# Optimization experiments

Hardware: AMD Instinct MI355X
Metric: run time of the kernel (lower is better)

Reference implementation:

```python
import jax, jax.numpy as jnp
import numpy as np

HEADS = 8
EPS = 1e-12  # F.normalize default eps


def conv1x1(t, w):
    # t: (B, Cin, H, W); w: (Cout, Cin) -> (B, Cout, H, W)
    return jnp.einsum('bchw,oc->bohw', t, w)


def cosine_attn(q, k, v, scale):
    # q: (B,h,d,Nq); k,v: (B,h,d,Nk). Cosine attention: L2-normalize over feature dim d.
    q = q / jnp.maximum(jnp.linalg.norm(q, axis=2, keepdims=True), EPS)
    k = k / jnp.maximum(jnp.linalg.norm(k, axis=2, keepdims=True), EPS)
    attn = jnp.einsum('bhdq,bhdk->bhqk', q, k) * scale
    attn = jax.nn.softmax(attn, axis=-1)
    return jnp.einsum('bhqk,bhdk->bhdq', attn, v)  # (B,h,d,Nq)


def setup_inputs() -> dict:
    key = jax.random.key(0)
    ks = jax.random.split(key, 8)
    B, C, H, W, L = 8, 512, 64, 64, 16
    def w(k, o, i):
        return jax.random.normal(k, (o, i), dtype=jnp.float32) * (1.0 / np.sqrt(i))
    return {
        'x': jax.random.normal(ks[0], (B, C, H, W), dtype=jnp.float32),
        'latents': jax.random.normal(ks[1], (1, C, 1, L), dtype=jnp.float32) * 0.02,
        'w_q_lat': w(ks[2], C, C),
        'w_kv_x': w(ks[3], 2 * C, C),
        'w_q_x': w(ks[4], C, C),
        'w_kv_lat': w(ks[5], 2 * C, C),
        'w_proj': w(ks[6], C, C),
        'b_proj': jnp.zeros((C,), dtype=jnp.float32),
    }


def reference(x, latents, w_q_lat, w_kv_x, w_q_x, w_kv_lat, w_proj, b_proj):
    B, C, H, W = x.shape
    L = latents.shape[-1]
    h = HEADS
    d = C // h
    scale = d ** (-0.5)

    # latents read from spatial features (compression)
    lat = jnp.broadcast_to(latents, (B, C, 1, L))
    ql = conv1x1(lat, w_q_lat).reshape(B, h, d, L)
    kvx = conv1x1(x, w_kv_x)
    kx = kvx[:, :C].reshape(B, h, d, H * W)
    vx = kvx[:, C:].reshape(B, h, d, H * W)
    lat_read = cosine_attn(ql, kx, vx, scale).reshape(B, C, 1, L)

    # latents write back into features (expansion)
    qx = conv1x1(x, w_q_x).reshape(B, h, d, H * W)
    kvl = conv1x1(lat_read, w_kv_lat)
    kl = kvl[:, :C].reshape(B, h, d, L)
    vl = kvl[:, C:].reshape(B, h, d, L)
    x_write = cosine_attn(qx, kl, vl, scale).reshape(B, C, H, W)

    # output projection (dropout p=0 -> identity)
    return conv1x1(x_write, w_proj) + b_proj[None, :, None, None]
```

## Files before the change

kernel.cpp:

```cpp
#include <hip/hip_runtime.h>


typedef __bf16 bf16x8 __attribute__((ext_vector_type(8)));
typedef float floatx4 __attribute__((ext_vector_type(4)));
typedef short short8_t __attribute__((ext_vector_type(8)));
typedef short short4_t __attribute__((ext_vector_type(4)));

#define DEV __device__ __forceinline__

DEV float bf2f(unsigned short u){ union{unsigned int i; float f;} v; v.i = ((unsigned int)u)<<16; return v.f; }
DEV unsigned short f2bf(float f){
  union{float f; unsigned int i;} v; v.f = f;
  unsigned int i = v.i;
  return (unsigned short)((i + 0x7fffu + ((i>>16)&1u)) >> 16);
}

#define OFF_XT     256ull
#define OFF_KVX    (OFF_XT + 33554432ull)
#define OFF_WKVX   (OFF_KVX + 67108864ull)
#define OFF_WQX    (OFF_WKVX + 1048576ull)
#define OFF_WKVL   (OFF_WQX + 524288ull)
#define OFF_WPROJ  (OFF_WKVL + 1048576ull)
#define OFF_WQLAT  (OFF_WPROJ + 524288ull)
#define OFF_LATF   (OFF_WQLAT + 524288ull)
#define OFF_BIAS   (OFF_LATF + 32768ull)
#define OFF_QL     (OFF_BIAS + 4096ull)
#define OFF_QLH    (OFF_QL + 32768ull)
#define OFF_GNUM   (OFF_QLH + 32768ull)
#define OFF_GDEN   (OFF_GNUM + 524288ull)
#define OFF_KVL    (OFF_GDEN + 4096ull)
#define OFF_KHAT   (OFF_KVL + 524288ull)
#define OFF_GVL    (OFF_KHAT + 524288ull)

__global__ void k_sniff(const unsigned short* __restrict__ x, int* flag){
  int t = threadIdx.x;
  int m = 0;
  for (int i = t; i < 4096; i += 256){ int e = (x[i]>>7)&0xFF; m = (e>m)?e:m; }
  __shared__ int red[256];
  red[t] = m; __syncthreads();
  for (int s = 128; s > 0; s >>= 1){ if (t < s) red[t] = (red[t+s]>red[t])?red[t+s]:red[t]; __syncthreads(); }
  if (t == 0) flag[0] = (red[0] > 150) ? 1 : 0;
}

__global__ __launch_bounds__(256) void k_cvt(const void* __restrict__ src, unsigned short* __restrict__ dst,
                                             int n, const int* __restrict__ flag){
  int base = (blockIdx.x*256 + threadIdx.x)*8;
  if (base >= n) return;
  if (*flag){
    const float* s = (const float*)src + base;
    float4 v0 = *(const float4*)(s);
    float4 v1 = *(const float4*)(s+4);
    unsigned short tmp[8] __attribute__((aligned(16)));
    tmp[0]=f2bf(v0.x); tmp[1]=f2bf(v0.y); tmp[2]=f2bf(v0.z); tmp[3]=f2bf(v0.w);
    tmp[4]=f2bf(v1.x); tmp[5]=f2bf(v1.y); tmp[6]=f2bf(v1.z); tmp[7]=f2bf(v1.w);
    *(short8_t*)&dst[base] = *(short8_t*)tmp;
  } else {
    *(short8_t*)&dst[base] = *(const short8_t*)((const unsigned short*)src + base);
  }
}

__global__ void k_cvtf(const void* __restrict__ src, float* __restrict__ dst, int n, const int* __restrict__ flag){
  int i = blockIdx.x*256 + threadIdx.x;
  if (i >= n) return;
  dst[i] = (*flag) ? ((const float*)src)[i] : bf2f(((const unsigned short*)src)[i]);
}

__global__ __launch_bounds__(256) void k_xt(const void* __restrict__ xraw, unsigned short* __restrict__ xT,
                                            const int* __restrict__ flag){
  int nb = blockIdx.x, cb = blockIdx.y, b = blockIdx.z;
  int n0 = nb*64, c0 = cb*64;
  __shared__ unsigned short tile[64][72];
  int t = threadIdx.x;
  if (*flag){
    const float* xp = (const float*)xraw;
#pragma unroll
    for (int i = 0; i < 4; ++i){
      int ch = i*256 + t; int c = ch>>4, n4 = (ch&15)*4;
      float4 v = *(const float4*)&xp[((size_t)(b*512 + c0 + c))*4096 + n0 + n4];
      int cc = n4 ^ (((c>>3)&7)<<3);
      tile[c][cc+0]=f2bf(v.x); tile[c][cc+1]=f2bf(v.y); tile[c][cc+2]=f2bf(v.z); tile[c][cc+3]=f2bf(v.w);
    }
  } else {
    const unsigned short* xp = (const unsigned short*)xraw;
#pragma unroll
    for (int i = 0; i < 2; ++i){
      int ch = i*256 + t; int c = ch>>3, n8 = (ch&7)*8;
      *(short8_t*)&tile[c][n8 ^ (((c>>3)&7)<<3)] =
        *(const short8_t*)&xp[((size_t)(b*512 + c0 + c))*4096 + n0 + n8];
    }
  }
  __syncthreads();
#pragma unroll
  for (int i = 0; i < 2; ++i){
    int ch = i*256 + t; int n = ch>>3, c8 = (ch&7)*8;
    unsigned short tmp[8] __attribute__((aligned(16)));
#pragma unroll
    for (int j = 0; j < 8; ++j){
      int c = c8 + j;
      tmp[j] = tile[c][n ^ (((c>>3)&7)<<3)];
    }
    *(short8_t*)&xT[((size_t)(b*4096 + n0 + n))*512 + c0 + c8] = *(short8_t*)tmp;
  }
}

__global__ __launch_bounds__(256) void k_ql(const unsigned short* __restrict__ wqlat,
                                            const float* __restrict__ latf, float* __restrict__ ql){
  int o0 = blockIdx.x*64;
  extern __shared__ char smr[];
  float* latb = (float*)smr;
  unsigned short* wt = (unsigned short*)(smr + 8192);
  int t = threadIdx.x;
  int o = t>>2, l4 = (t&3)*4;
  float acc[4] = {0.f,0.f,0.f,0.f};
  for (int kk = 0; kk < 512; kk += 128){
    __syncthreads();
#pragma unroll
    for (int j = 0; j < 8; ++j){ int i = j*256 + t; latb[i] = latf[kk*16 + i]; }
#pragma unroll
    for (int j = 0; j < 4; ++j){ int ch = j*256 + t; int r = ch>>4, kc = (ch&15)*8;
      *(short8_t*)&wt[r*136 + kc] = *(const short8_t*)&wqlat[(size_t)(o0+r)*512 + kk + kc]; }
    __syncthreads();
    for (int k = 0; k < 128; ++k){
      float w = bf2f(wt[o*136 + k]);
      const float* lr = &latb[k*16 + l4];
#pragma unroll
      for (int j = 0; j < 4; ++j) acc[j] += w*lr[j];
    }
  }
#pragma unroll
  for (int j = 0; j < 4; ++j) ql[(o0+o)*16 + l4 + j] = acc[j];
}

__global__ void k_qlnorm(const float* __restrict__ ql, float* __restrict__ qlh){
  int l = blockIdx.x, h = blockIdx.y, d = threadIdx.x;
  float v = ql[(h*64 + d)*16 + l];
  float ss = v*v;
  for (int off = 32; off; off >>= 1) ss += __shfl_xor(ss, off);
  qlh[(h*16 + l)*64 + d] = 0.125f * v / fmaxf(sqrtf(ss), 1e-12f);
}

DEV void gemm128(const unsigned short* __restrict__ Ap0, const unsigned short* __restrict__ Ap1,
                 const unsigned short* __restrict__ Bp,
                 unsigned short* At, unsigned short* Bt, floatx4 (&acc)[4][4]){
  int t = threadIdx.x, lane = t&63, wave = t>>6;
  int wm = wave>>1, wn = wave&1, lr = lane&15, lq = lane>>4;
  for (int kk = 0; kk < 512; kk += 64){
    __syncthreads();
#pragma unroll
    for (int i = 0; i < 4; ++i){
      int ch = i*256 + t; int r = ch>>3, kc = (ch&7)*8;
      const unsigned short* ap = (i < 2) ? (Ap0 + (size_t)r*512) : (Ap1 + (size_t)(r-64)*512);
      *(short8_t*)&At[r*72 + kc] = *(const short8_t*)&ap[kk + kc];
    }
#pragma unroll
    for (int i = 0; i < 4; ++i){
      int ch = i*256 + t; int r = ch>>3, kc = (ch&7)*8;
      *(short8_t*)&Bt[r*72 + kc] = *(const short8_t*)&Bp[(size_t)r*512 + kk + kc];
    }
    __syncthreads();
#pragma unroll
    for (int ks = 0; ks < 2; ++ks){
      bf16x8 a[4], b[4];
#pragma unroll
      for (int mt = 0; mt < 4; ++mt) a[mt] = *(const bf16x8*)&At[(wm*64 + mt*16 + lr)*72 + ks*32 + lq*8];
#pragma unroll
      for (int nt = 0; nt < 4; ++nt) b[nt] = *(const bf16x8*)&Bt[(wn*64 + nt*16 + lr)*72 + ks*32 + lq*8];
#pragma unroll
      for (int mt = 0; mt < 4; ++mt)
#pragma unroll
        for (int nt = 0; nt < 4; ++nt)
          acc[mt][nt] = __builtin_amdgcn_mfma_f32_16x16x32_bf16(a[mt], b[nt], acc[mt][nt], 0, 0, 0);
    }
  }
  __syncthreads();
}

__global__ __launch_bounds__(256) void k_kvattn1(const unsigned short* __restrict__ wkvx,
                                                 const unsigned short* __restrict__ xT,
                                                 const float* __restrict__ qlh2,
                                                 float* __restrict__ gnum, float* __restrict__ gden){
  int nb = blockIdx.x, h = blockIdx.y, b = blockIdx.z;
  int n0 = nb*128;
  extern __shared__ char smr[];
  unsigned short* At  = (unsigned short*)smr;
  unsigned short* Bt  = At + 128*72;
  unsigned short* kt  = At;
  unsigned short* vt  = Bt;
  unsigned short* qls = (unsigned short*)(smr + 36864);
  float* ssq  = (float*)(smr + 39168);
  float* wred = (float*)(smr + 39680);
  unsigned short* pt  = (unsigned short*)(smr + 39936);
  int t = threadIdx.x, lane = t&63, wave = t>>6;
  int wm = wave>>1, wn = wave&1, lr = lane&15, lq = lane>>4;
  floatx4 acc[4][4];
  floatx4 zero = {0.f,0.f,0.f,0.f};
#pragma unroll
  for (int i = 0; i < 4; ++i) for (int j = 0; j < 4; ++j) acc[i][j] = zero;
  gemm128(wkvx + (size_t)(h*64)*512, wkvx + (size_t)(512 + h*64)*512,
          xT + ((size_t)(b*4096 + n0))*512, At, Bt, acc);
  for (int i = t; i < 1024; i += 256) qls[(i>>6)*72 + (i&63)] = f2bf(qlh2[(size_t)h*1024 + i]);
  if (wm == 0){
#pragma unroll
    for (int nt = 0; nt < 4; ++nt){
      float s = 0.f;
#pragma unroll
      for (int mt = 0; mt < 4; ++mt)
#pragma unroll
        for (int r = 0; r < 4; ++r) s += acc[mt][nt][r]*acc[mt][nt][r];
      s += __shfl_xor(s, 16); s += __shfl_xor(s, 32);
      if (lq == 0) ssq[wn*64 + nt*16 + lr] = 1.f / fmaxf(sqrtf(s), 1e-12f);
    }
  } else {
#pragma unroll
    for (int mt = 0; mt < 4; ++mt)
#pragma unroll
      for (int nt = 0; nt < 4; ++nt){
        int col = wn*64 + nt*16 + lr;
#pragma unroll
        for (int r = 0; r < 4; ++r) vt[(mt*16 + lq*4 + r)*136 + col] = f2bf(acc[mt][nt][r]);
      }
  }
  __syncthreads();
  if (wm == 0){
#pragma unroll
    for (int nt = 0; nt < 4; ++nt){
      int col = wn*64 + nt*16 + lr;
      float rinv = ssq[col];
#pragma unroll
      for (int mt = 0; mt < 4; ++mt){
        unsigned short tmp[4] __attribute__((aligned(8)));
#pragma unroll
        for (int r = 0; r < 4; ++r) tmp[r] = f2bf(acc[mt][nt][r]*rinv);
        *(short4_t*)&kt[col*72 + mt*16 + lq*4] = *(short4_t*)tmp;
      }
    }
  }
  __syncthreads();
  floatx4 sl[2]; sl[0] = zero; sl[1] = zero;
#pragma unroll
  for (int ks = 0; ks < 2; ++ks){
    bf16x8 bb = *(const bf16x8*)&qls[lr*72 + ks*32 + lq*8];
#pragma unroll
    for (int i = 0; i < 2; ++i){
      bf16x8 aa = *(const bf16x8*)&kt[((wave*2 + i)*16 + lr)*72 + ks*32 + lq*8];
      sl[i] = __builtin_amdgcn_mfma_f32_16x16x32_bf16(aa, bb, sl[i], 0, 0, 0);
    }
  }
  float dp = 0.f;
  float pv[2][4];
#pragma unroll
  for (int i = 0; i < 2; ++i)
#pragma unroll
    for (int r = 0; r < 4; ++r){ float p = __expf(sl[i][r]); pv[i][r] = p; dp += p; }
  dp += __shfl_xor(dp, 16); dp += __shfl_xor(dp, 32);
  if (lq == 0) wred[wave*16 + lr] = dp;
#pragma unroll
  for (int i = 0; i < 2; ++i){
    unsigned short tmp[4] __attribute__((aligned(8)));
#pragma unroll
    for (int r = 0; r < 4; ++r) tmp[r] = f2bf(pv[i][r]);
    *(short4_t*)&pt[lr*136 + (wave*2 + i)*16 + lq*4] = *(short4_t*)tmp;
  }
  __syncthreads();
  int bh = b*8 + h;
  if (t < 16) atomicAdd(&gden[bh*16 + t], wred[t] + wred[16+t] + wred[32+t] + wred[48+t]);
  floatx4 nacc = zero;
#pragma unroll
  for (int ks = 0; ks < 4; ++ks){
    bf16x8 aa = *(const bf16x8*)&vt[(wave*16 + lr)*136 + ks*32 + lq*8];
    bf16x8 bb = *(const bf16x8*)&pt[lr*136 + ks*32 + lq*8];
    nacc = __builtin_amdgcn_mfma_f32_16x16x32_bf16(aa, bb, nacc, 0, 0, 0);
  }
  float* gp = &gnum[((size_t)bh*16 + lr)*64 + wave*16 + lq*4];
#pragma unroll
  for (int r = 0; r < 4; ++r) atomicAdd(&gp[r], nacc[r]);
}

__global__ __launch_bounds__(256) void k_kvl(const unsigned short* __restrict__ wkvl,
                                             const float* __restrict__ gnum, const float* __restrict__ gden,
                                             float* __restrict__ kvl){
  int ob = blockIdx.x, b = blockIdx.y;
  extern __shared__ char smr[];
  float* latb = (float*)smr;
  unsigned short* wt = (unsigned short*)(smr + 32768);
  int t = threadIdx.x;
  for (int i = t; i < 8192; i += 256){
    int c = i>>4, l = i&15;
    int h = c>>6, d = c&63;
    int bh = b*8 + h;
    latb[i] = gnum[((size_t)(bh*16 + l))*64 + d] / gden[bh*16 + l];
  }
  int o = t>>4, l = t&15;
  int o0 = ob*16;
  float acc = 0.f;
  for (int kk = 0; kk < 512; kk += 128){
    __syncthreads();
    { int r = t>>4, kc = (t&15)*8;
      *(short8_t*)&wt[r*136 + kc] = *(const short8_t*)&wkvl[(size_t)(o0+r)*512 + kk + kc]; }
    __syncthreads();
    for (int k = 0; k < 128; ++k) acc += bf2f(wt[o*136 + k]) * latb[(kk+k)*16 + l];
  }
  kvl[((size_t)(b*1024 + o0 + o))*16 + l] = acc;
}

__global__ void k_klnorm(const float* __restrict__ kvl, float* __restrict__ khat, float* __restrict__ gvl){
  int l = blockIdx.x, h = blockIdx.y, b = blockIdx.z, d = threadIdx.x;
  float kl = kvl[((size_t)(b*1024 + h*64 + d))*16 + l];
  float vl = kvl[((size_t)(b*1024 + 512 + h*64 + d))*16 + l];
  float ss = kl*kl;
  for (int off = 32; off; off >>= 1) ss += __shfl_xor(ss, off);
  float inv = 0.125f / fmaxf(sqrtf(ss), 1e-12f);
  size_t o = ((size_t)((b*8+h)*16 + l))*64 + d;
  khat[o] = kl*inv;
  gvl[o] = vl;
}

__global__ __launch_bounds__(256) void k_mmat(const unsigned short* __restrict__ wproj,
                                              const float* __restrict__ gvl,
                                              unsigned short* __restrict__ Mg){
  int cb = blockIdx.x, h = blockIdx.y, b = blockIdx.z;
  __shared__ unsigned short wt[128*68];
  int t = threadIdx.x;
#pragma unroll
  for (int i = 0; i < 4; ++i){ int ch = i*256 + t; int c = ch>>3, d8 = (ch&7)*8;
    *(short8_t*)&wt[c*68 + d8] = *(const short8_t*)&wproj[(size_t)(cb*128 + c)*512 + h*64 + d8]; }
  int l = t&15, cq = t>>4;
  float v[64];
  const float* vp = &gvl[((size_t)(b*8+h)*16 + l)*64];
#pragma unroll
  for (int j = 0; j < 16; ++j){ float4 f = *(const float4*)&vp[j*4];
    v[j*4+0]=f.x; v[j*4+1]=f.y; v[j*4+2]=f.z; v[j*4+3]=f.w; }
  __syncthreads();
#pragma unroll
  for (int c8 = 0; c8 < 8; ++c8){
    int c = cq*8 + c8;
    float dot = 0.f;
#pragma unroll
    for (int d = 0; d < 64; ++d) dot += bf2f(wt[c*68 + d]) * v[d];
    Mg[((size_t)(b*512) + cb*128 + c)*128 + h*16 + l] = f2bf(dot);
  }
}

__global__ __launch_bounds__(256) void k_attn2p2(const unsigned short* __restrict__ wqx,
                                                 const unsigned short* __restrict__ xT,
                                                 const float* __restrict__ khatg,
                                                 unsigned short* __restrict__ Pg){
  int nb = blockIdx.x, hp = blockIdx.y, b = blockIdx.z;
  int n0 = nb*128;
  extern __shared__ char smr[];
  unsigned short* At  = (unsigned short*)smr;
  unsigned short* Bt  = At + 128*72;
  unsigned short* qt0 = At;
  unsigned short* qt1 = Bt;
  unsigned short* khs = (unsigned short*)(smr + 36864);
  float* ssq = (float*)(smr + 41472);
  int t = threadIdx.x, lane = t&63, wave = t>>6;
  int wm = wave>>1, wn = wave&1, lr = lane&15, lq = lane>>4;
  floatx4 acc[4][4];
  floatx4 zero = {0.f,0.f,0.f,0.f};
#pragma unroll
  for (int i = 0; i < 4; ++i) for (int j = 0; j < 4; ++j) acc[i][j] = zero;
  gemm128(wqx + (size_t)(hp*128)*512, wqx + (size_t)(hp*128 + 64)*512,
          xT + ((size_t)(b*4096 + n0))*512, At, Bt, acc);
  for (int i = t; i < 2048; i += 256){
    int hh = i>>10, rem = i&1023;
    khs[hh*1152 + (rem>>6)*72 + (rem&63)] = f2bf(khatg[((size_t)(b*8 + hp*2 + hh))*1024 + rem]);
  }
#pragma unroll
  for (int nt = 0; nt < 4; ++nt){
    float s = 0.f;
#pragma unroll
    for (int mt = 0; mt < 4; ++mt)
#pragma unroll
      for (int r = 0; r < 4; ++r) s += acc[mt][nt][r]*acc[mt][nt][r];
    s += __shfl_xor(s, 16); s += __shfl_xor(s, 32);
    if (lq == 0) ssq[wm*128 + wn*64 + nt*16 + lr] = 1.f / fmaxf(sqrtf(s), 1e-12f);
  }
  __syncthreads();
  unsigned short* qtr = wm ? qt1 : qt0;
#pragma unroll
  for (int nt = 0; nt < 4; ++nt){
    int col = wn*64 + nt*16 + lr;
    float rinv = ssq[wm*128 + col];
#pragma unroll
    for (int mt = 0; mt < 4; ++mt){
      unsigned short tmp[4] __attribute__((aligned(8)));
#pragma unroll
      for (int r = 0; r < 4; ++r) tmp[r] = f2bf(acc[mt][nt][r]*rinv);
      *(short4_t*)&qtr[col*72 + mt*16 + lq*4] = *(short4_t*)tmp;
    }
  }
  __syncthreads();
  floatx4 sl[4];
#pragma unroll
  for (int i = 0; i < 4; ++i) sl[i] = zero;
#pragma unroll
  for (int ks = 0; ks < 2; ++ks){
    bf16x8 bb = *(const bf16x8*)&khs[wm*1152 + lr*72 + ks*32 + lq*8];
#pragma unroll
    for (int i = 0; i < 4; ++i){
      bf16x8 aa = *(const bf16x8*)&qtr[((wn*4 + i)*16 + lr)*72 + ks*32 + lq*8];
      sl[i] = __builtin_amdgcn_mfma_f32_16x16x32_bf16(aa, bb, sl[i], 0, 0, 0);
    }
  }
  int h = hp*2 + wm;
#pragma unroll
  for (int i = 0; i < 4; ++i){
    float p[4], s[4];
#pragma unroll
    for (int r = 0; r < 4; ++r){ p[r] = __expf(sl[i][r]); s[r] = p[r]; }
#pragma unroll
    for (int r = 0; r < 4; ++r){
      s[r] += __shfl_xor(s[r], 1);
      s[r] += __shfl_xor(s[r], 2);
      s[r] += __shfl_xor(s[r], 4);
      s[r] += __shfl_xor(s[r], 8);
    }
    int nbase = wn*64 + i*16 + lq*4;
#pragma unroll
    for (int r = 0; r < 4; ++r)
      Pg[((size_t)(b*4096 + n0 + nbase + r))*128 + h*16 + lr] = f2bf(p[r]/s[r]);
  }
}

__global__ __launch_bounds__(256) void k_out(const unsigned short* __restrict__ Mg,
                                             const unsigned short* __restrict__ Pg,
                                             const float* __restrict__ biasf,
                                             void* __restrict__ outv, const int* __restrict__ flag){
  int nb = blockIdx.x, cb = blockIdx.y, b = blockIdx.z;
  int n0 = nb*128, c0 = cb*64;
  extern __shared__ char smr[];
  unsigned short* At = (unsigned short*)smr;
  unsigned short* Bt = At + 64*136;
  int t = threadIdx.x, lane = t&63, wave = t>>6;
  int wm = wave>>1, wn = wave&1, lr = lane&15, lq = lane>>4;
#pragma unroll
  for (int i = 0; i < 4; ++i){ int ch = i*256 + t; int r = ch>>4, p8 = (ch&15)*8;
    *(short8_t*)&At[r*136 + p8] = *(const short8_t*)&Mg[((size_t)(b*512 + c0 + r))*128 + p8]; }
#pragma unroll
  for (int i = 0; i < 8; ++i){ int ch = i*256 + t; int r = ch>>4, p8 = (ch&15)*8;
    *(short8_t*)&Bt[r*136 + p8] = *(const short8_t*)&Pg[((size_t)(b*4096 + n0 + r))*128 + p8]; }
  __syncthreads();
  floatx4 acc[2][4];
  floatx4 zero = {0.f,0.f,0.f,0.f};
#pragma unroll
  for (int i = 0; i < 2; ++i) for (int j = 0; j < 4; ++j) acc[i][j] = zero;
#pragma unroll
  for (int ks = 0; ks < 4; ++ks){
    bf16x8 a0 = *(const bf16x8*)&At[(wm*32 + lr)*136 + ks*32 + lq*8];
    bf16x8 a1 = *(const bf16x8*)&At[(wm*32 + 16 + lr)*136 + ks*32 + lq*8];
#pragma unroll
    for (int nt = 0; nt < 4; ++nt){
      bf16x8 bb = *(const bf16x8*)&Bt[(wn*64 + nt*16 + lr)*136 + ks*32 + lq*8];
      acc[0][nt] = __builtin_amdgcn_mfma_f32_16x16x32_bf16(a0, bb, acc[0][nt], 0, 0, 0);
      acc[1][nt] = __builtin_amdgcn_mfma_f32_16x16x32_bf16(a1, bb, acc[1][nt], 0, 0, 0);
    }
  }
  __syncthreads();
  float* ct = (float*)smr;
#pragma unroll
  for (int mt = 0; mt < 2; ++mt)
#pragma unroll
    for (int nt = 0; nt < 4; ++nt)
#pragma unroll
      for (int r = 0; r < 4; ++r){
        int row = wm*32 + mt*16 + lq*4 + r;
        ct[row*132 + wn*64 + nt*16 + lr] = acc[mt][nt][r] + biasf[c0 + row];
      }
  __syncthreads();
  if (*flag){
    float* of = (float*)outv;
#pragma unroll
    for (int i = 0; i < 8; ++i){ int ch = i*256 + t; int r = ch>>5, c4 = (ch&31)*4;
      *(float4*)&of[((size_t)(b*512 + c0 + r))*4096 + n0 + c4] = *(float4*)&ct[r*132 + c4]; }
  } else {
    unsigned short* ob = (unsigned short*)outv;
#pragma unroll
    for (int i = 0; i < 4; ++i){ int ch = i*256 + t; int r = ch>>4, c8 = (ch&15)*8;
      unsigned short tmp[8] __attribute__((aligned(16)));
#pragma unroll
      for (int j = 0; j < 8; ++j) tmp[j] = f2bf(ct[r*132 + c8 + j]);
      *(short8_t*)&ob[((size_t)(b*512 + c0 + r))*4096 + n0 + c8] = *(short8_t*)tmp; }
  }
}

extern "C" void kernel_launch(void* const* d_in, const int* in_sizes, int n_in,
                              void* d_out, int out_size, void* d_ws, size_t ws_size,
                              hipStream_t stream){
  (void)in_sizes; (void)n_in; (void)out_size; (void)ws_size;
  char* ws = (char*)d_ws;
  int* flag              = (int*)ws;
  unsigned short* xT     = (unsigned short*)(ws + OFF_XT);
  unsigned short* Pg     = (unsigned short*)(ws + OFF_KVX);
  unsigned short* Mg     = (unsigned short*)(ws + OFF_KVX + 8388608ull);
  unsigned short* wkvx   = (unsigned short*)(ws + OFF_WKVX);
  unsigned short* wqx    = (unsigned short*)(ws + OFF_WQX);
  unsigned short* wkvl   = (unsigned short*)(ws + OFF_WKVL);
  unsigned short* wproj  = (unsigned short*)(ws + OFF_WPROJ);
  unsigned short* wqlat  = (unsigned short*)(ws + OFF_WQLAT);
  float* latf  = (float*)(ws + OFF_LATF);
  float* biasf = (float*)(ws + OFF_BIAS);
  float* ql    = (float*)(ws + OFF_QL);
  float* qlh   = (float*)(ws + OFF_QLH);
  float* gnum  = (float*)(ws + OFF_GNUM);
  float* gden  = (float*)(ws + OFF_GDEN);
  float* kvl   = (float*)(ws + OFF_KVL);
  float* khat  = (float*)(ws + OFF_KHAT);
  float* gvl   = (float*)(ws + OFF_GVL);

  k_sniff<<<1, 256, 0, stream>>>((const unsigned short*)d_in[0], flag);

  k_cvt<<<256, 256, 0, stream>>>(d_in[3], wkvx, 524288, flag);
  k_cvt<<<128, 256, 0, stream>>>(d_in[4], wqx,  262144, flag);
  k_cvt<<<256, 256, 0, stream>>>(d_in[5], wkvl, 524288, flag);
  k_cvt<<<128, 256, 0, stream>>>(d_in[6], wproj,262144, flag);
  k_cvt<<<128, 256, 0, stream>>>(d_in[2], wqlat,262144, flag);
  k_cvtf<<<32, 256, 0, stream>>>(d_in[1], latf, 8192, flag);
  k_cvtf<<<2, 256, 0, stream>>>(d_in[7], biasf, 512, flag);

  k_xt<<<dim3(64, 8, 8), 256, 0, stream>>>(d_in[0], xT, flag);

  k_ql<<<8, 256, 8192 + 64*136*2, stream>>>(wqlat, latf, ql);
  k_qlnorm<<<dim3(16, 8), 64, 0, stream>>>(ql, qlh);

  hipMemsetAsync(ws + OFF_GNUM, 0, 524288 + 4096, stream);

  k_kvattn1<<<dim3(32, 8, 8), 256, 44288, stream>>>(wkvx, xT, qlh, gnum, gden);
  k_kvl<<<dim3(64, 8), 256, 32768 + 16*136*2, stream>>>(wkvl, gnum, gden, kvl);
  k_klnorm<<<dim3(16, 8, 8), 64, 0, stream>>>(kvl, khat, gvl);
  k_mmat<<<dim3(4, 8, 8), 256, 0, stream>>>(wproj, gvl, Mg);
  k_attn2p2<<<dim3(32, 4, 8), 256, 42496, stream>>>(wqx, xT, khat, Pg);
  k_out<<<dim3(32, 8, 8), 256, 52224, stream>>>(Mg, Pg, biasf, d_out, flag);
}
```

Baseline: 314.8 us.

## Use direct global-to-LDS loads in GEMM tiles and merge prep kernels

The shared 128x128 GEMM tile loader now uses global_load_lds 16-byte transfers, which write straight into LDS without going through registers, and the padded stride is dropped to an unpadded 64-element row. The shared-memory layouts of the kernels that use it are rebased to match. The seven weight, latent and bias conversion launches are folded into a single k_prep kernel, and the query-latent normalization is fused into k_ql, so several small launches go away. The unpadded LDS rows can bring back bank conflicts on the MFMA fragment reads, and any inconsistency in the new offsets would be a correctness risk.

```diff
diff --git a/kernel.cpp b/kernel.cpp
--- a/kernel.cpp
+++ b/kernel.cpp
@@ -13,6 +13,11 @@
   union{float f; unsigned int i;} v; v.f = f;
   unsigned int i = v.i;
   return (unsigned short)((i + 0x7fffu + ((i>>16)&1u)) >> 16);
+}
+
+DEV void glds16(const void* g, void* l){
+  __builtin_amdgcn_global_load_lds((const __attribute__((address_space(1))) void*)g,
+                                   (__attribute__((address_space(3))) void*)l, 16, 0, 0);
 }
 
 #define OFF_XT     256ull
@@ -24,8 +29,7 @@
 #define OFF_WQLAT  (OFF_WPROJ + 524288ull)
 #define OFF_LATF   (OFF_WQLAT + 524288ull)
 #define OFF_BIAS   (OFF_LATF + 32768ull)
-#define OFF_QL     (OFF_BIAS + 4096ull)
-#define OFF_QLH    (OFF_QL + 32768ull)
+#define OFF_QLH    (OFF_BIAS + 4096ull)
 #define OFF_GNUM   (OFF_QLH + 32768ull)
 #define OFF_GDEN   (OFF_GNUM + 524288ull)
 #define OFF_KVL    (OFF_GDEN + 4096ull)
@@ -42,27 +46,41 @@
   if (t == 0) flag[0] = (red[0] > 150) ? 1 : 0;
 }
 
-__global__ __launch_bounds__(256) void k_cvt(const void* __restrict__ src, unsigned short* __restrict__ dst,
-                                             int n, const int* __restrict__ flag){
-  int base = (blockIdx.x*256 + threadIdx.x)*8;
-  if (base >= n) return;
-  if (*flag){
-    const float* s = (const float*)src + base;
-    float4 v0 = *(const float4*)(s);
-    float4 v1 = *(const float4*)(s+4);
-    unsigned short tmp[8] __attribute__((aligned(16)));
-    tmp[0]=f2bf(v0.x); tmp[1]=f2bf(v0.y); tmp[2]=f2bf(v0.z); tmp[3]=f2bf(v0.w);
-    tmp[4]=f2bf(v1.x); tmp[5]=f2bf(v1.y); tmp[6]=f2bf(v1.z); tmp[7]=f2bf(v1.w);
-    *(short8_t*)&dst[base] = *(short8_t*)tmp;
+__global__ __launch_bounds__(256) void k_prep(const void* s0, const void* s1, const void* s2,
+                                              const void* s3, const void* s4,
+                                              const void* slat, const void* sbias,
+                                              unsigned short* __restrict__ wdst,
+                                              float* __restrict__ latf, float* __restrict__ biasf,
+                                              const int* __restrict__ flag){
+  int b = blockIdx.x, t = threadIdx.x;
+  int isf = *flag;
+  if (b < 896){
+    int e = b*2048 + t*8;
+    const void* src; int off;
+    if (e < 524288)      { src = s0; off = e; }
+    else if (e < 786432) { src = s1; off = e - 524288; }
+    else if (e < 1310720){ src = s2; off = e - 786432; }
+    else if (e < 1572864){ src = s3; off = e - 1310720; }
+    else                 { src = s4; off = e - 1572864; }
+    if (isf){
+      const float* s = (const float*)src + off;
+      float4 v0 = *(const float4*)(s);
+      float4 v1 = *(const float4*)(s+4);
+      unsigned short tmp[8] __attribute__((aligned(16)));
+      tmp[0]=f2bf(v0.x); tmp[1]=f2bf(v0.y); tmp[2]=f2bf(v0.z); tmp[3]=f2bf(v0.w);
+      tmp[4]=f2bf(v1.x); tmp[5]=f2bf(v1.y); tmp[6]=f2bf(v1.z); tmp[7]=f2bf(v1.w);
+      *(short8_t*)&wdst[e] = *(short8_t*)tmp;
+    } else {
+      *(short8_t*)&wdst[e] = *(const short8_t*)((const unsigned short*)src + off);
+    }
+  } else if (b < 900){
+    int i = (b-896)*2048 + t*8;
+#pragma unroll
+    for (int j = 0; j < 8; ++j)
+      latf[i+j] = isf ? ((const float*)slat)[i+j] : bf2f(((const unsigned short*)slat)[i+j]);
   } else {
-    *(short8_t*)&dst[base] = *(const short8_t*)((const unsigned short*)src + base);
-  }
-}
-
-__global__ void k_cvtf(const void* __restrict__ src, float* __restrict__ dst, int n, const int* __restrict__ flag){
-  int i = blockIdx.x*256 + threadIdx.x;
-  if (i >= n) return;
-  dst[i] = (*flag) ? ((const float*)src)[i] : bf2f(((const unsigned short*)src)[i]);
+    if (t < 512) biasf[t] = isf ? ((const float*)sbias)[t] : bf2f(((const unsigned short*)sbias)[t]);
+  }
 }
 
 __global__ __launch_bounds__(256) void k_xt(const void* __restrict__ xraw, unsigned short* __restrict__ xT,
@@ -104,11 +122,13 @@
 }
 
 __global__ __launch_bounds__(256) void k_ql(const unsigned short* __restrict__ wqlat,
-                                            const float* __restrict__ latf, float* __restrict__ ql){
-  int o0 = blockIdx.x*64;
+                                            const float* __restrict__ latf, float* __restrict__ qlh){
+  int h = blockIdx.x, o0 = h*64;
   extern __shared__ char smr[];
   float* latb = (float*)smr;
   unsigned short* wt = (unsigned short*)(smr + 8192);
+  float* qbuf = (float*)(smr + 8192 + 17408);
+  float* rinv = (float*)(smr + 8192 + 17408 + 4096);
   int t = threadIdx.x;
   int o = t>>2, l4 = (t&3)*4;
   float acc[4] = {0.f,0.f,0.f,0.f};
@@ -128,15 +148,16 @@
     }
   }
 #pragma unroll
-  for (int j = 0; j < 4; ++j) ql[(o0+o)*16 + l4 + j] = acc[j];
-}
-
-__global__ void k_qlnorm(const float* __restrict__ ql, float* __restrict__ qlh){
-  int l = blockIdx.x, h = blockIdx.y, d = threadIdx.x;
-  float v = ql[(h*64 + d)*16 + l];
-  float ss = v*v;
-  for (int off = 32; off; off >>= 1) ss += __shfl_xor(ss, off);
-  qlh[(h*16 + l)*64 + d] = 0.125f * v / fmaxf(sqrtf(ss), 1e-12f);
+  for (int j = 0; j < 4; ++j) qbuf[o*16 + l4 + j] = acc[j];
+  __syncthreads();
+  if (t < 16){
+    float ss = 0.f;
+    for (int oo = 0; oo < 64; ++oo){ float v = qbuf[oo*16 + t]; ss += v*v; }
+    rinv[t] = 0.125f / fmaxf(sqrtf(ss), 1e-12f);
+  }
+  __syncthreads();
+#pragma unroll
+  for (int j = 0; j < 4; ++j) qlh[(h*16 + l4 + j)*64 + o] = acc[j]*rinv[l4 + j];
 }
 
 DEV void gemm128(const unsigned short* __restrict__ Ap0, const unsigned short* __restrict__ Ap1,
@@ -144,27 +165,32 @@
                  unsigned short* At, unsigned short* Bt, floatx4 (&acc)[4][4]){
   int t = threadIdx.x, lane = t&63, wave = t>>6;
   int wm = wave>>1, wn = wave&1, lr = lane&15, lq = lane>>4;
+  int rsub = lane>>3;
+  int koff = (lane&7)*8;
   for (int kk = 0; kk < 512; kk += 64){
     __syncthreads();
 #pragma unroll
-    for (int i = 0; i < 4; ++i){
-      int ch = i*256 + t; int r = ch>>3, kc = (ch&7)*8;
-      const unsigned short* ap = (i < 2) ? (Ap0 + (size_t)r*512) : (Ap1 + (size_t)(r-64)*512);
-      *(short8_t*)&At[r*72 + kc] = *(const short8_t*)&ap[kk + kc];
-    }
-#pragma unroll
-    for (int i = 0; i < 4; ++i){
-      int ch = i*256 + t; int r = ch>>3, kc = (ch&7)*8;
-      *(short8_t*)&Bt[r*72 + kc] = *(const short8_t*)&Bp[(size_t)r*512 + kk + kc];
+    for (int c2 = 0; c2 < 4; ++c2){
+      int chunk = wave*4 + c2;
+      int row = chunk*8 + rsub;
+      const unsigned short* gp = (chunk < 8) ? (Ap0 + (size_t)row*512 + kk + koff)
+                                             : (Ap1 + (size_t)(row-64)*512 + kk + koff);
+      glds16(gp, At + chunk*512);
+    }
+#pragma unroll
+    for (int c2 = 0; c2 < 4; ++c2){
+      int chunk = wave*4 + c2;
+      int row = chunk*8 + rsub;
+      glds16(Bp + (size_t)row*512 + kk + koff, Bt + chunk*512);
     }
     __syncthreads();
 #pragma unroll
     for (int ks = 0; ks < 2; ++ks){
       bf16x8 a[4], b[4];
 #pragma unroll
-      for (int mt = 0; mt < 4; ++mt) a[mt] = *(const bf16x8*)&At[(wm*64 + mt*16 + lr)*72 + ks*32 + lq*8];
-#pragma unroll
-      for (int nt = 0; nt < 4; ++nt) b[nt] = *(const bf16x8*)&Bt[(wn*64 + nt*16 + lr)*72 + ks*32 + lq*8];
+      for (int mt = 0; mt < 4; ++mt) a[mt] = *(const bf16x8*)&At[(wm*64 + mt*16 + lr)*64 + ks*32 + lq*8];
+#pragma unroll
+      for (int nt = 0; nt < 4; ++nt) b[nt] = *(const bf16x8*)&Bt[(wn*64 + nt*16 + lr)*64 + ks*32 + lq*8];
 #pragma unroll
       for (int mt = 0; mt < 4; ++mt)
 #pragma unroll
@@ -183,13 +209,13 @@
   int n0 = nb*128;
   extern __shared__ char smr[];
   unsigned short* At  = (unsigned short*)smr;
-  unsigned short* Bt  = At + 128*72;
-  unsigned short* kt  = At;
-  unsigned short* vt  = Bt;
-  unsigned short* qls = (unsigned short*)(smr + 36864);
-  float* ssq  = (float*)(smr + 39168);
-  float* wred = (float*)(smr + 39680);
-  unsigned short* pt  = (unsigned short*)(smr + 39936);
+  unsigned short* Bt  = (unsigned short*)(smr + 16384);
+  unsigned short* kt  = (unsigned short*)smr;
+  unsigned short* vt  = (unsigned short*)(smr + 18432);
+  unsigned short* qls = (unsigned short*)(smr + 35840);
+  float* ssq  = (float*)(smr + 38144);
+  float* wred = (float*)(smr + 38656);
+  unsigned short* pt  = (unsigned short*)(smr + 38912);
   int t = threadIdx.x, lane = t&63, wave = t>>6;
   int wm = wave>>1, wn = wave&1, lr = lane&15, lq = lane>>4;
   floatx4 acc[4][4];
@@ -349,9 +375,9 @@
   int n0 = nb*128;
   extern __shared__ char smr[];
   unsigned short* At  = (unsigned short*)smr;
-  unsigned short* Bt  = At + 128*72;
-  unsigned short* qt0 = At;
-  unsigned short* qt1 = Bt;
+  unsigned short* Bt  = (unsigned short*)(smr + 16384);
+  unsigned short* qt0 = (unsigned short*)smr;
+  unsigned short* qt1 = (unsigned short*)(smr + 18432);
   unsigned short* khs = (unsigned short*)(smr + 36864);
   float* ssq = (float*)(smr + 41472);
   int t = threadIdx.x, lane = t&63, wave = t>>6;
@@ -394,12 +420,13 @@
   floatx4 sl[4];
 #pragma unroll
   for (int i = 0; i < 4; ++i) sl[i] = zero;
+  unsigned short* qsrc = wm ? qt1 : qt0;
 #pragma unroll
   for (int ks = 0; ks < 2; ++ks){
     bf16x8 bb = *(const bf16x8*)&khs[wm*1152 + lr*72 + ks*32 + lq*8];
 #pragma unroll
     for (int i = 0; i < 4; ++i){
-      bf16x8 aa = *(const bf16x8*)&qtr[((wn*4 + i)*16 + lr)*72 + ks*32 + lq*8];
+      bf16x8 aa = *(const bf16x8*)&qsrc[((wn*4 + i)*16 + lr)*72 + ks*32 + lq*8];
       sl[i] = __builtin_amdgcn_mfma_f32_16x16x32_bf16(aa, bb, sl[i], 0, 0, 0);
     }
   }
@@ -497,10 +524,8 @@
   unsigned short* wqx    = (unsigned short*)(ws + OFF_WQX);
   unsigned short* wkvl   = (unsigned short*)(ws + OFF_WKVL);
   unsigned short* wproj  = (unsigned short*)(ws + OFF_WPROJ);
-  unsigned short* wqlat  = (unsigned short*)(ws + OFF_WQLAT);
   float* latf  = (float*)(ws + OFF_LATF);
   float* biasf = (float*)(ws + OFF_BIAS);
-  float* ql    = (float*)(ws + OFF_QL);
   float* qlh   = (float*)(ws + OFF_QLH);
   float* gnum  = (float*)(ws + OFF_GNUM);
   float* gden  = (float*)(ws + OFF_GDEN);
@@ -510,22 +535,16 @@
 
   k_sniff<<<1, 256, 0, stream>>>((const unsigned short*)d_in[0], flag);
 
-  k_cvt<<<256, 256, 0, stream>>>(d_in[3], wkvx, 524288, flag);
-  k_cvt<<<128, 256, 0, stream>>>(d_in[4], wqx,  262144, flag);
-  k_cvt<<<256, 256, 0, stream>>>(d_in[5], wkvl, 524288, flag);
-  k_cvt<<<128, 256, 0, stream>>>(d_in[6], wproj,262144, flag);
-  k_cvt<<<128, 256, 0, stream>>>(d_in[2], wqlat,262144, flag);
-  k_cvtf<<<32, 256, 0, stream>>>(d_in[1], latf, 8192, flag);
-  k_cvtf<<<2, 256, 0, stream>>>(d_in[7], biasf, 512, flag);
+  k_prep<<<901, 256, 0, stream>>>(d_in[3], d_in[4], d_in[5], d_in[6], d_in[2],
+                                  d_in[1], d_in[7], wkvx, latf, biasf, flag);
 
   k_xt<<<dim3(64, 8, 8), 256, 0, stream>>>(d_in[0], xT, flag);
 
-  k_ql<<<8, 256, 8192 + 64*136*2, stream>>>(wqlat, latf, ql);
-  k_qlnorm<<<dim3(16, 8), 64, 0, stream>>>(ql, qlh);
+  k_ql<<<8, 256, 8192 + 17408 + 4096 + 64, stream>>>((unsigned short*)(ws + OFF_WQLAT), latf, qlh);
 
   hipMemsetAsync(ws + OFF_GNUM, 0, 524288 + 4096, stream);
 
-  k_kvattn1<<<dim3(32, 8, 8), 256, 44288, stream>>>(wkvx, xT, qlh, gnum, gden);
+  k_kvattn1<<<dim3(32, 8, 8), 256, 43264, stream>>>(wkvx, xT, qlh, gnum, gden);
   k_kvl<<<dim3(64, 8), 256, 32768 + 16*136*2, stream>>>(wkvl, gnum, gden, kvl);
   k_klnorm<<<dim3(16, 8, 8), 64, 0, stream>>>(kvl, khat, gvl);
   k_mmat<<<dim3(4, 8, 8), 256, 0, stream>>>(wproj, gvl, Mg);
```

Result: no change. 310.5 us (-1.4%).
